# Optimization experiments

Measured on AMD Instinct MI355X. Metric: run time of the kernel, lower is better.

Reference implementation:

```python
import jax, jax.numpy as jnp
import numpy as np

EMBED_DIM = 1024
Q_DIM = 512
KV_DIM = 512
NUM_HEADS = 16
HEAD_DIM = EMBED_DIM // NUM_HEADS
EPS = 1e-5


def setup_inputs() -> dict:
    key = jax.random.key(0)
    ks = jax.random.split(key, 13)
    B, N1, N2 = 2, 2048, 2048
    s_q = 1.0 / np.sqrt(Q_DIM)
    s_kv = 1.0 / np.sqrt(KV_DIM)
    s_e = 1.0 / np.sqrt(EMBED_DIM)
    return {
        "query": jax.random.normal(ks[0], (B, N1, Q_DIM), jnp.float32),
        "key": jax.random.normal(ks[1], (B, N2, KV_DIM), jnp.float32),
        "value": jax.random.normal(ks[2], (B, N2, KV_DIM), jnp.float32),
        "Wq": jax.random.uniform(ks[3], (Q_DIM, EMBED_DIM), jnp.float32, -s_q, s_q),
        "bq": jax.random.uniform(ks[4], (EMBED_DIM,), jnp.float32, -s_q, s_q),
        "Wk": jax.random.uniform(ks[5], (KV_DIM, EMBED_DIM), jnp.float32, -s_kv, s_kv),
        "bk": jax.random.uniform(ks[6], (EMBED_DIM,), jnp.float32, -s_kv, s_kv),
        "Wv": jax.random.uniform(ks[7], (KV_DIM, EMBED_DIM), jnp.float32, -s_kv, s_kv),
        "bv": jax.random.uniform(ks[8], (EMBED_DIM,), jnp.float32, -s_kv, s_kv),
        "Wo": jax.random.uniform(ks[9], (EMBED_DIM, EMBED_DIM), jnp.float32, -s_e, s_e),
        "bo": jax.random.uniform(ks[10], (EMBED_DIM,), jnp.float32, -s_e, s_e),
        "gamma": jnp.ones((EMBED_DIM,), jnp.float32),
        "beta": jnp.zeros((EMBED_DIM,), jnp.float32),
    }


def reference(query, key, value, Wq, bq, Wk, bk, Wv, bv, Wo, bo, gamma, beta):
    B, N1, _ = query.shape
    _, N2, _ = key.shape
    scale = HEAD_DIM ** (-0.5)
    # projections -> [B, H, N, D]
    Q = (query @ Wq + bq).reshape(B, N1, NUM_HEADS, HEAD_DIM).transpose(0, 2, 1, 3)
    K = (key @ Wk + bk).reshape(B, N2, NUM_HEADS, HEAD_DIM).transpose(0, 2, 1, 3)
    V = (value @ Wv + bv).reshape(B, N2, NUM_HEADS, HEAD_DIM).transpose(0, 2, 1, 3)
    # full score matrix [B, H, N1, N2] (matches original eager attention)
    att = jnp.einsum("bhqd,bhkd->bhqk", Q, K) * scale
    att = jax.nn.softmax(att, axis=-1)
    # dropout is identity in eval mode
    out = jnp.einsum("bhqk,bhkd->bhqd", att, V)  # [B, H, N1, D]
    out = out.transpose(0, 2, 1, 3).reshape(B, N1, EMBED_DIM)
    out = out @ Wo + bo
    # LayerNorm
    mu = out.mean(-1, keepdims=True)
    var = ((out - mu) ** 2).mean(-1, keepdims=True)
    return (out - mu) * jax.lax.rsqrt(var + EPS) * gamma + beta
```

## Files before the change

kernel.cpp:

```cpp
#include <hip/hip_runtime.h>

typedef __bf16 bf16x8 __attribute__((ext_vector_type(8)));
typedef __bf16 bf16x4 __attribute__((ext_vector_type(4)));
typedef __bf16 bf16x2 __attribute__((ext_vector_type(2)));
typedef float f32x4 __attribute__((ext_vector_type(4)));
typedef unsigned short u16;
typedef unsigned int u32;

__device__ __forceinline__ f32x4 mfma16(bf16x8 a, bf16x8 b, f32x4 c) {
  return __builtin_amdgcn_mfma_f32_16x16x32_bf16(a, b, c, 0, 0, 0);
}

__device__ __forceinline__ void gload_lds16(const void* g, void* l) {
  __builtin_amdgcn_global_load_lds(
      (const __attribute__((address_space(1))) void*)g,
      (__attribute__((address_space(3))) void*)l, 16, 0, 0);
}

__device__ __forceinline__ void swap32(u32& a, u32& b) {
  asm volatile("v_permlane32_swap_b32 %0, %1" : "+v"(a), "+v"(b));
}
__device__ __forceinline__ void swap16(u32& a, u32& b) {
  asm volatile("v_permlane16_swap_b32 %0, %1" : "+v"(a), "+v"(b));
}

__device__ __forceinline__ u32 pkbf(float a, float b) {
  union { bf16x2 h; u32 w; } u;
  u.h[0] = (__bf16)a;
  u.h[1] = (__bf16)b;
  return u.w;
}

__global__ __launch_bounds__(256) void prep(const float4* __restrict__ qi,
                                            const float4* __restrict__ ki,
                                            const float4* __restrict__ vi,
                                            bf16x4* __restrict__ oq,
                                            bf16x4* __restrict__ ok,
                                            bf16x4* __restrict__ ov,
                                            const float* __restrict__ W0,
                                            const float* __restrict__ W1,
                                            const float* __restrict__ W2,
                                            const float* __restrict__ W3,
                                            u16* __restrict__ T0, u16* __restrict__ T1,
                                            u16* __restrict__ T2, u16* __restrict__ T3,
                                            int n4) {
  const int z = blockIdx.y;
  const int tid = threadIdx.x;
  if (z < 3) {
    int i = blockIdx.x * 256 + tid;
    if (i >= n4) return;
    const float4* in = z == 0 ? qi : z == 1 ? ki : vi;
    bf16x4* out = z == 0 ? oq : z == 1 ? ok : ov;
    float4 v = in[i];
    bf16x4 o;
    o[0] = (__bf16)v.x; o[1] = (__bf16)v.y; o[2] = (__bf16)v.z; o[3] = (__bf16)v.w;
    out[i] = o;
  } else {
    const int zz = z - 3;
    const int K = (zz == 3) ? 1024 : 512;
    const int nb = (K / 32) * 32;
    if (blockIdx.x >= nb) return;
    const float* W = zz == 0 ? W0 : zz == 1 ? W1 : zz == 2 ? W2 : W3;
    u16* Wt = zz == 0 ? T0 : zz == 1 ? T1 : zz == 2 ? T2 : T3;
    __shared__ float t[32][33];
    const int tx = tid & 31, ty = tid >> 5;
    const int n0 = (blockIdx.x & 31) * 32, k0 = (blockIdx.x >> 5) * 32;
#pragma unroll
    for (int i = 0; i < 4; ++i)
      t[ty + i * 8][tx] = W[(size_t)(k0 + ty + i * 8) * 1024 + n0 + tx];
    __syncthreads();
#pragma unroll
    for (int i = 0; i < 4; ++i)
      ((__bf16*)Wt)[(size_t)(n0 + ty + i * 8) * K + k0 + tx] = (__bf16)t[tx][ty + i * 8];
  }
}

template <int MODE, int DBUF>
__device__ __forceinline__ void gemm_body(const u16* __restrict__ A,
                                          const u16* __restrict__ Bt,
                                          const float* __restrict__ bias,
                                          void* __restrict__ Cout,
                                          int M, int N, int K, float scl) {
  constexpr int NB = DBUF ? 2 : 1;
  __shared__ __align__(16) u16 lA[NB][128 * 64];
  __shared__ __align__(16) u16 lB[NB][128 * 64];
  const int tid = threadIdx.x;
  const int w = tid >> 6, l = tid & 63;
  const int li = l & 15, lg = l >> 4;
  const int wm = w & 1, wn = w >> 1;
  const int bm = blockIdx.x * 128, bn = blockIdx.y * 128;

  f32x4 acc[4][4] = {};
  const int nk = K >> 6;

  auto stage = [&](int kt, int bufi) {
    const int k0 = kt << 6;
#pragma unroll
    for (int i = 0; i < 4; ++i) {
      const int c0 = (i * 4 + w) * 64;
      const int f = c0 + l;
      const int r = f >> 3, cs = (f & 7) ^ (r & 7);
      gload_lds16(A + (size_t)(bm + r) * K + k0 + cs * 8, &lA[bufi][c0 * 8]);
      gload_lds16(Bt + (size_t)(bn + r) * K + k0 + cs * 8, &lB[bufi][c0 * 8]);
    }
  };

  int cur = 0;
  if (DBUF) {
    stage(0, 0);
    __syncthreads();
  }

  for (int kt = 0; kt < nk; ++kt) {
    if (DBUF) {
      if (kt + 1 < nk) stage(kt + 1, cur ^ 1);
    } else {
      stage(kt, 0);
      __syncthreads();
    }
    bf16x8 af[4][2], bfr[4][2];
#pragma unroll
    for (int m = 0; m < 4; ++m) {
      const int row = wm * 64 + m * 16 + li;
#pragma unroll
      for (int kk = 0; kk < 2; ++kk) {
        const int kc = (lg + kk * 4) ^ (row & 7);
        af[m][kk] = *(const bf16x8*)&lA[cur][row * 64 + kc * 8];
      }
    }
#pragma unroll
    for (int n = 0; n < 4; ++n) {
      const int row = wn * 64 + n * 16 + li;
#pragma unroll
      for (int kk = 0; kk < 2; ++kk) {
        const int kc = (lg + kk * 4) ^ (row & 7);
        bfr[n][kk] = *(const bf16x8*)&lB[cur][row * 64 + kc * 8];
      }
    }
#pragma unroll
    for (int m = 0; m < 4; ++m)
#pragma unroll
      for (int n = 0; n < 4; ++n) {
        acc[m][n] = mfma16(af[m][0], bfr[n][0], acc[m][n]);
        acc[m][n] = mfma16(af[m][1], bfr[n][1], acc[m][n]);
      }
    __syncthreads();
    if (DBUF) cur ^= 1;
  }

#pragma unroll
  for (int m = 0; m < 4; ++m) {
    const int row0 = bm + wm * 64 + m * 16 + lg * 4;
#pragma unroll
    for (int n = 0; n < 4; ++n) {
      const int col = bn + wn * 64 + n * 16 + li;
      const float bv = bias[col];
      if (MODE == 2) {
        const int bq = row0 >> 11, kv = row0 & 2047;
        bf16x4 pk;
#pragma unroll
        for (int r = 0; r < 4; ++r) pk[r] = (__bf16)((acc[m][n][r] + bv) * scl);
        *(bf16x4*)&((u16*)Cout)[((size_t)(bq * 1024 + col)) * 2048 + kv] = pk;
      } else {
#pragma unroll
        for (int r = 0; r < 4; ++r) {
          float v = (acc[m][n][r] + bv) * scl;
          ((__bf16*)Cout)[(size_t)(row0 + r) * N + col] = (__bf16)v;
        }
      }
    }
  }
}

__global__ __launch_bounds__(256) void gemm_qkv(const u16* __restrict__ xq,
                                                const u16* __restrict__ xk,
                                                const u16* __restrict__ xv,
                                                const u16* __restrict__ wqt,
                                                const u16* __restrict__ wkt,
                                                const u16* __restrict__ wvt,
                                                const float* __restrict__ bq,
                                                const float* __restrict__ bk,
                                                const float* __restrict__ bv,
                                                u16* __restrict__ Qb, u16* __restrict__ Kb,
                                                u16* __restrict__ Vt, float qscale) {
  const int z = blockIdx.z;
  if (z == 0) {
    gemm_body<0, 0>(xq, wqt, bq, Qb, 4096, 1024, 512, qscale);
  } else if (z == 1) {
    gemm_body<0, 0>(xk, wkt, bk, Kb, 4096, 1024, 512, 1.0f);
  } else {
    gemm_body<2, 0>(xv, wvt, bv, Vt, 4096, 1024, 512, 1.0f);
  }
}

__global__ __launch_bounds__(512) void gemm_o8(const u16* __restrict__ A,
                                               const u16* __restrict__ Bt,
                                               const float* __restrict__ bias,
                                               u16* __restrict__ C) {
  constexpr int N = 1024, K = 1024;
  __shared__ __align__(16) u16 lA[2][128 * 64];
  __shared__ __align__(16) u16 lB[2][128 * 64];
  const int tid = threadIdx.x;
  const int w = tid >> 6, l = tid & 63;
  const int li = l & 15, lg = l >> 4;
  const int wm = w & 1, wn = w >> 1;
  const int bm = blockIdx.x * 128, bn = blockIdx.y * 128;

  f32x4 acc[4][2] = {};
  const int nk = K >> 6;

  auto stage = [&](int kt, int bufi) {
    const int k0 = kt << 6;
#pragma unroll
    for (int i = 0; i < 2; ++i) {
      const int c0 = (i * 8 + w) * 64;
      const int f = c0 + l;
      const int r = f >> 3, cs = (f & 7) ^ (r & 7);
      gload_lds16(A + (size_t)(bm + r) * K + k0 + cs * 8, &lA[bufi][c0 * 8]);
      gload_lds16(Bt + (size_t)(bn + r) * K + k0 + cs * 8, &lB[bufi][c0 * 8]);
    }
  };

  int cur = 0;
  stage(0, 0);
  __syncthreads();

  for (int kt = 0; kt < nk; ++kt) {
    if (kt + 1 < nk) stage(kt + 1, cur ^ 1);
    bf16x8 af[4][2], bfr[2][2];
#pragma unroll
    for (int m = 0; m < 4; ++m) {
      const int row = wm * 64 + m * 16 + li;
#pragma unroll
      for (int kk = 0; kk < 2; ++kk) {
        const int kc = (lg + kk * 4) ^ (row & 7);
        af[m][kk] = *(const bf16x8*)&lA[cur][row * 64 + kc * 8];
      }
    }
#pragma unroll
    for (int n = 0; n < 2; ++n) {
      const int row = wn * 32 + n * 16 + li;
#pragma unroll
      for (int kk = 0; kk < 2; ++kk) {
        const int kc = (lg + kk * 4) ^ (row & 7);
        bfr[n][kk] = *(const bf16x8*)&lB[cur][row * 64 + kc * 8];
      }
    }
#pragma unroll
    for (int m = 0; m < 4; ++m)
#pragma unroll
      for (int n = 0; n < 2; ++n) {
        acc[m][n] = mfma16(af[m][0], bfr[n][0], acc[m][n]);
        acc[m][n] = mfma16(af[m][1], bfr[n][1], acc[m][n]);
      }
    __syncthreads();
    cur ^= 1;
  }

#pragma unroll
  for (int m = 0; m < 4; ++m) {
    const int row0 = bm + wm * 64 + m * 16 + lg * 4;
#pragma unroll
    for (int n = 0; n < 2; ++n) {
      const int col = bn + wn * 32 + n * 16 + li;
      const float bv = bias[col];
#pragma unroll
      for (int r = 0; r < 4; ++r)
        ((__bf16*)C)[(size_t)(row0 + r) * N + col] = (__bf16)(acc[m][n][r] + bv);
    }
  }
}

__global__ __launch_bounds__(512, 4) void attn64(const u16* __restrict__ Qb,
                                                 const u16* __restrict__ Kb,
                                                 const u16* __restrict__ Vt,
                                                 u16* __restrict__ Opart,
                                                 float* __restrict__ Lpart,
                                                 int N1, int N2) {
  const int tid = threadIdx.x;
  const int w = tid >> 6, l = tid & 63;
  const int li = l & 15, lg = l >> 4;

  const int flat = blockIdx.x + 8 * (blockIdx.y + 16 * blockIdx.z);
  const int xcd = flat & 7, idx = flat >> 3;
  const int qb = idx & 7, rest = idx >> 3;
  const int h = 2 * xcd + (rest & 1);
  const int b = (rest >> 1) & 1;
  const int kvh = rest >> 2;
  const int q0 = qb * 256;

  __shared__ __align__(16) u16 lK[4][64 * 64];
  __shared__ __align__(16) u16 lV[4][64 * 64];

  bf16x8 qa[2][2];
#pragma unroll
  for (int s = 0; s < 2; ++s) {
    const size_t qoff = (size_t)(b * N1 + q0 + s * 128 + w * 16 + li) * 1024 + h * 64;
    qa[s][0] = *(const bf16x8*)&Qb[qoff + lg * 8];
    qa[s][1] = *(const bf16x8*)&Qb[qoff + 32 + lg * 8];
  }

  const u16* Kbase = Kb + (size_t)b * N2 * 1024 + h * 64;
  const u16* Vbase = Vt + (size_t)((b * 16 + h) * 64) * N2;

  const int sr = tid >> 3;
  const int sc = (tid & 7) ^ (sr & 7);

  f32x4 o[2][4] = {};
  float lsum0 = 0.f, lsum1 = 0.f;
  const int ca = lg ^ (li & 7), cb = (lg + 4) ^ (li & 7);

  auto stageK = [&](int t, int bufi) {
    gload_lds16(Kbase + (size_t)(t * 64 + sr) * 1024 + sc * 8, &lK[bufi][w * 512]);
  };
  auto stageV = [&](int t, int bufi) {
    gload_lds16(Vbase + (size_t)sr * N2 + t * 64 + sc * 8, &lV[bufi][w * 512]);
  };

  auto tile_body = [&](const u16* K_, const u16* V_) {
    float st0 = 0.f, st1 = 0.f;
    u32 u0[4][2], u1[4][2];
    __builtin_amdgcn_s_setprio(1);
#pragma unroll
    for (int n = 0; n < 4; ++n) {
      const int row = n * 16 + li;
      bf16x8 k0 = *(const bf16x8*)&K_[row * 64 + ca * 8];
      bf16x8 k1 = *(const bf16x8*)&K_[row * 64 + cb * 8];
      f32x4 a = {}, a2 = {};
      a = mfma16(k0, qa[0][0], a);
      a = mfma16(k1, qa[0][1], a);
      a2 = mfma16(k0, qa[1][0], a2);
      a2 = mfma16(k1, qa[1][1], a2);
      float p0 = __builtin_amdgcn_exp2f(a[0]);
      float p1 = __builtin_amdgcn_exp2f(a[1]);
      float p2 = __builtin_amdgcn_exp2f(a[2]);
      float p3 = __builtin_amdgcn_exp2f(a[3]);
      st0 += (p0 + p1) + (p2 + p3);
      u0[n][0] = pkbf(p0, p1);
      u0[n][1] = pkbf(p2, p3);
      float r0 = __builtin_amdgcn_exp2f(a2[0]);
      float r1 = __builtin_amdgcn_exp2f(a2[1]);
      float r2 = __builtin_amdgcn_exp2f(a2[2]);
      float r3 = __builtin_amdgcn_exp2f(a2[3]);
      st1 += (r0 + r1) + (r2 + r3);
      u1[n][0] = pkbf(r0, r1);
      u1[n][1] = pkbf(r2, r3);
    }
    __builtin_amdgcn_s_setprio(0);
    lsum0 += st0;
    lsum1 += st1;

#pragma unroll
    for (int c = 0; c < 2; ++c) {
      swap32(u0[0][c], u0[1][c]); swap32(u0[2][c], u0[3][c]);
      swap32(u1[0][c], u1[1][c]); swap32(u1[2][c], u1[3][c]);
    }
#pragma unroll
    for (int c = 0; c < 2; ++c) {
      swap16(u0[0][c], u0[1][c]); swap16(u0[2][c], u0[3][c]);
      swap16(u1[0][c], u1[1][c]); swap16(u1[2][c], u1[3][c]);
    }

    __builtin_amdgcn_s_setprio(1);
#pragma unroll
    for (int ks = 0; ks < 2; ++ks) {
      union { u32 w4[4]; bf16x8 v; } f0, f1;
      f0.w4[0] = u0[2 * ks][0]; f0.w4[1] = u0[2 * ks][1];
      f0.w4[2] = u0[2 * ks + 1][0]; f0.w4[3] = u0[2 * ks + 1][1];
      f1.w4[0] = u1[2 * ks][0]; f1.w4[1] = u1[2 * ks][1];
      f1.w4[2] = u1[2 * ks + 1][0]; f1.w4[3] = u1[2 * ks + 1][1];
#pragma unroll
      for (int dt = 0; dt < 4; ++dt) {
        const int row = dt * 16 + li;
        const int c = (lg + ks * 4) ^ (li & 7);
        const bf16x8 vf = *(const bf16x8*)&V_[row * 64 + c * 8];
        o[0][dt] = mfma16(vf, f0.v, o[0][dt]);
        o[1][dt] = mfma16(vf, f1.v, o[1][dt]);
      }
    }
    __builtin_amdgcn_s_setprio(0);
  };

  const int t0 = kvh * 16;

  stageK(t0, 0); stageV(t0, 0);
  stageK(t0 + 1, 1); stageV(t0 + 1, 1);
  __syncthreads();

  for (int tt = 0; tt < 16; tt += 2) {
    const int t = t0 + tt;
    if (tt + 2 < 16) { stageK(t + 2, (tt + 2) & 3); stageV(t + 2, (tt + 2) & 3); }
    if (tt + 3 < 16) { stageK(t + 3, (tt + 3) & 3); stageV(t + 3, (tt + 3) & 3); }
    tile_body(lK[tt & 3], lV[tt & 3]);
    tile_body(lK[(tt + 1) & 3], lV[(tt + 1) & 3]);
    __syncthreads();
  }

  lsum0 += __shfl_xor(lsum0, 16, 64);
  lsum0 += __shfl_xor(lsum0, 32, 64);
  lsum1 += __shfl_xor(lsum1, 16, 64);
  lsum1 += __shfl_xor(lsum1, 32, 64);

  u16* Op = Opart + (size_t)kvh * 4096 * 1024;
#pragma unroll
  for (int s = 0; s < 2; ++s) {
    const int qrow = b * N1 + q0 + s * 128 + w * 16 + li;
    const size_t orow = (size_t)qrow * 1024 + h * 64;
#pragma unroll
    for (int dt = 0; dt < 4; ++dt) {
      bf16x4 pk;
#pragma unroll
      for (int r = 0; r < 4; ++r) pk[r] = (__bf16)o[s][dt][r];
      *(bf16x4*)&Op[orow + dt * 16 + lg * 4] = pk;
    }
    if (lg == 0)
      Lpart[(size_t)kvh * 4096 * 16 + (size_t)qrow * 16 + h] = (s == 0 ? lsum0 : lsum1);
  }
}

__global__ __launch_bounds__(256) void combine(const u16* __restrict__ Opart,
                                               const float* __restrict__ Lpart,
                                               u16* __restrict__ ao) {
  const int row = blockIdx.x;
  const int tid = threadIdx.x;
  const int h = tid >> 4;
  const float l = Lpart[(size_t)row * 16 + h] + Lpart[4096 * 16 + (size_t)row * 16 + h];
  const float inv = 1.f / l;
  const size_t off = (size_t)row * 1024 + tid * 4;
  const bf16x4 a = *(const bf16x4*)&Opart[off];
  const bf16x4 b = *(const bf16x4*)&Opart[(size_t)4096 * 1024 + off];
  bf16x4 o;
#pragma unroll
  for (int j = 0; j < 4; ++j) o[j] = (__bf16)(((float)a[j] + (float)b[j]) * inv);
  *(bf16x4*)&ao[off] = o;
}

__global__ __launch_bounds__(256) void lnorm(const u16* __restrict__ X,
                                             const float* __restrict__ gamma,
                                             const float* __restrict__ beta,
                                             float* __restrict__ out) {
  const int row = blockIdx.x;
  const int tid = threadIdx.x;
  const bf16x4 xv = ((const bf16x4*)(X + (size_t)row * 1024))[tid];
  float4 v;
  v.x = (float)xv[0]; v.y = (float)xv[1]; v.z = (float)xv[2]; v.w = (float)xv[3];
  float s = v.x + v.y + v.z + v.w;
  float sq = v.x * v.x + v.y * v.y + v.z * v.z + v.w * v.w;
#pragma unroll
  for (int d = 1; d < 64; d <<= 1) {
    s += __shfl_xor(s, d, 64);
    sq += __shfl_xor(sq, d, 64);
  }
  __shared__ float red[8];
  const int w = tid >> 6, l = tid & 63;
  if (l == 0) { red[w] = s; red[4 + w] = sq; }
  __syncthreads();
  s = red[0] + red[1] + red[2] + red[3];
  sq = red[4] + red[5] + red[6] + red[7];
  const float mu = s * (1.f / 1024.f);
  const float var = sq * (1.f / 1024.f) - mu * mu;
  const float rstd = rsqrtf(var + 1e-5f);
  const float4 g = ((const float4*)gamma)[tid];
  const float4 bb = ((const float4*)beta)[tid];
  float4 o;
  o.x = (v.x - mu) * rstd * g.x + bb.x;
  o.y = (v.y - mu) * rstd * g.y + bb.y;
  o.z = (v.z - mu) * rstd * g.z + bb.z;
  o.w = (v.w - mu) * rstd * g.w + bb.w;
  ((float4*)(out + (size_t)row * 1024))[tid] = o;
}

extern "C" void kernel_launch(void* const* d_in, const int* in_sizes, int n_in,
                              void* d_out, int out_size, void* d_ws, size_t ws_size,
                              hipStream_t stream) {
  const float* query = (const float*)d_in[0];
  const float* key_ = (const float*)d_in[1];
  const float* value = (const float*)d_in[2];
  const float* Wq = (const float*)d_in[3];
  const float* bq = (const float*)d_in[4];
  const float* Wk = (const float*)d_in[5];
  const float* bk = (const float*)d_in[6];
  const float* Wv = (const float*)d_in[7];
  const float* bv = (const float*)d_in[8];
  const float* Wo = (const float*)d_in[9];
  const float* bo = (const float*)d_in[10];
  const float* gamma = (const float*)d_in[11];
  const float* beta = (const float*)d_in[12];

  constexpr int B = 2, N1 = 2048, N2 = 2048, E = 1024, QKD = 512;
  constexpr int M = B * N1;
  const float QSCALE = 0.125f * 1.4426950408889634f;

  char* p = (char*)d_ws;
  auto alloc = [&](size_t bytes) {
    char* r = p;
    p += (bytes + 255) & ~(size_t)255;
    return r;
  };
  u16* xq = (u16*)alloc((size_t)M * QKD * 2);
  u16* xk = (u16*)alloc((size_t)M * QKD * 2);
  u16* xv = (u16*)alloc((size_t)M * QKD * 2);
  u16* wqt = (u16*)alloc((size_t)E * QKD * 2);
  u16* wkt = (u16*)alloc((size_t)E * QKD * 2);
  u16* wvt = (u16*)alloc((size_t)E * QKD * 2);
  u16* wot = (u16*)alloc((size_t)E * E * 2);
  u16* Qb = (u16*)alloc((size_t)M * E * 2);
  u16* Kb = (u16*)alloc((size_t)M * E * 2);
  u16* Vt = (u16*)alloc((size_t)M * E * 2);
  u16* ao = (u16*)alloc((size_t)M * E * 2);
  u16* ao2 = (u16*)alloc((size_t)M * E * 2);
  u16* Opart = (u16*)alloc((size_t)2 * M * E * 2);
  float* Lpart = (float*)alloc((size_t)2 * M * 16 * 4);

  const int n4 = M * QKD / 4;
  prep<<<dim3((n4 + 255) / 256, 7), 256, 0, stream>>>(
      (const float4*)query, (const float4*)key_, (const float4*)value,
      (bf16x4*)xq, (bf16x4*)xk, (bf16x4*)xv,
      Wq, Wk, Wv, Wo, wqt, wkt, wvt, wot, n4);

  gemm_qkv<<<dim3(M / 128, E / 128, 3), 256, 0, stream>>>(
      xq, xk, xv, wqt, wkt, wvt, bq, bk, bv, Qb, Kb, Vt, QSCALE);

  attn64<<<dim3(8, 16, 4), 512, 0, stream>>>(Qb, Kb, Vt, Opart, Lpart, N1, N2);

  combine<<<M, 256, 0, stream>>>(Opart, Lpart, ao);

  gemm_o8<<<dim3(M / 128, E / 128), 512, 0, stream>>>(ao, wot, bo, ao2);

  lnorm<<<M, 256, 0, stream>>>(ao2, gamma, beta, (float*)d_out);
}
```

Before: 103.6 us.

## Fuse split-KV combine into output GEMM and use 8-wave double-buffered QKV GEMM

The separate combine kernel is removed. The output-projection GEMM now loads both partial attention outputs and their softmax denominators, sums and normalizes them in registers, and writes the A tile into LDS while B is still staged asynchronously. The QKV projection GEMM moves to 512 threads with 8 waves and double-buffered LDS, matching the output GEMM. This saves one launch and a full round trip through the intermediate activation buffer. In exchange it adds register pressure and global-to-register loads on the output GEMM's A path.

```diff
diff --git a/kernel.cpp b/kernel.cpp
--- a/kernel.cpp
+++ b/kernel.cpp
@@ -75,29 +75,28 @@
   }
 }
 
-template <int MODE, int DBUF>
-__device__ __forceinline__ void gemm_body(const u16* __restrict__ A,
-                                          const u16* __restrict__ Bt,
-                                          const float* __restrict__ bias,
-                                          void* __restrict__ Cout,
-                                          int M, int N, int K, float scl) {
-  constexpr int NB = DBUF ? 2 : 1;
-  __shared__ __align__(16) u16 lA[NB][128 * 64];
-  __shared__ __align__(16) u16 lB[NB][128 * 64];
+template <int MODE>
+__device__ __forceinline__ void gemm8_body(const u16* __restrict__ A,
+                                           const u16* __restrict__ Bt,
+                                           const float* __restrict__ bias,
+                                           u16* __restrict__ Cout,
+                                           int N, int K, float scl) {
+  __shared__ __align__(16) u16 lA[2][128 * 64];
+  __shared__ __align__(16) u16 lB[2][128 * 64];
   const int tid = threadIdx.x;
   const int w = tid >> 6, l = tid & 63;
   const int li = l & 15, lg = l >> 4;
   const int wm = w & 1, wn = w >> 1;
   const int bm = blockIdx.x * 128, bn = blockIdx.y * 128;
 
-  f32x4 acc[4][4] = {};
+  f32x4 acc[4][2] = {};
   const int nk = K >> 6;
 
   auto stage = [&](int kt, int bufi) {
     const int k0 = kt << 6;
 #pragma unroll
-    for (int i = 0; i < 4; ++i) {
-      const int c0 = (i * 4 + w) * 64;
+    for (int i = 0; i < 2; ++i) {
+      const int c0 = (i * 8 + w) * 64;
       const int f = c0 + l;
       const int r = f >> 3, cs = (f & 7) ^ (r & 7);
       gload_lds16(A + (size_t)(bm + r) * K + k0 + cs * 8, &lA[bufi][c0 * 8]);
@@ -106,19 +105,12 @@
   };
 
   int cur = 0;
-  if (DBUF) {
-    stage(0, 0);
-    __syncthreads();
-  }
+  stage(0, 0);
+  __syncthreads();
 
   for (int kt = 0; kt < nk; ++kt) {
-    if (DBUF) {
-      if (kt + 1 < nk) stage(kt + 1, cur ^ 1);
-    } else {
-      stage(kt, 0);
-      __syncthreads();
-    }
-    bf16x8 af[4][2], bfr[4][2];
+    if (kt + 1 < nk) stage(kt + 1, cur ^ 1);
+    bf16x8 af[4][2], bfr[2][2];
 #pragma unroll
     for (int m = 0; m < 4; ++m) {
       const int row = wm * 64 + m * 16 + li;
@@ -129,8 +121,8 @@
       }
     }
 #pragma unroll
-    for (int n = 0; n < 4; ++n) {
-      const int row = wn * 64 + n * 16 + li;
+    for (int n = 0; n < 2; ++n) {
+      const int row = wn * 32 + n * 16 + li;
 #pragma unroll
       for (int kk = 0; kk < 2; ++kk) {
         const int kc = (lg + kk * 4) ^ (row & 7);
@@ -140,60 +132,61 @@
 #pragma unroll
     for (int m = 0; m < 4; ++m)
 #pragma unroll
-      for (int n = 0; n < 4; ++n) {
+      for (int n = 0; n < 2; ++n) {
         acc[m][n] = mfma16(af[m][0], bfr[n][0], acc[m][n]);
         acc[m][n] = mfma16(af[m][1], bfr[n][1], acc[m][n]);
       }
     __syncthreads();
-    if (DBUF) cur ^= 1;
+    cur ^= 1;
   }
 
 #pragma unroll
   for (int m = 0; m < 4; ++m) {
     const int row0 = bm + wm * 64 + m * 16 + lg * 4;
 #pragma unroll
-    for (int n = 0; n < 4; ++n) {
-      const int col = bn + wn * 64 + n * 16 + li;
+    for (int n = 0; n < 2; ++n) {
+      const int col = bn + wn * 32 + n * 16 + li;
       const float bv = bias[col];
       if (MODE == 2) {
         const int bq = row0 >> 11, kv = row0 & 2047;
         bf16x4 pk;
 #pragma unroll
         for (int r = 0; r < 4; ++r) pk[r] = (__bf16)((acc[m][n][r] + bv) * scl);
-        *(bf16x4*)&((u16*)Cout)[((size_t)(bq * 1024 + col)) * 2048 + kv] = pk;
+        *(bf16x4*)&Cout[((size_t)(bq * 1024 + col)) * 2048 + kv] = pk;
       } else {
 #pragma unroll
-        for (int r = 0; r < 4; ++r) {
-          float v = (acc[m][n][r] + bv) * scl;
-          ((__bf16*)Cout)[(size_t)(row0 + r) * N + col] = (__bf16)v;
-        }
-      }
-    }
-  }
-}
-
-__global__ __launch_bounds__(256) void gemm_qkv(const u16* __restrict__ xq,
-                                                const u16* __restrict__ xk,
-                                                const u16* __restrict__ xv,
-                                                const u16* __restrict__ wqt,
-                                                const u16* __restrict__ wkt,
-                                                const u16* __restrict__ wvt,
-                                                const float* __restrict__ bq,
-                                                const float* __restrict__ bk,
-                                                const float* __restrict__ bv,
-                                                u16* __restrict__ Qb, u16* __restrict__ Kb,
-                                                u16* __restrict__ Vt, float qscale) {
+        for (int r = 0; r < 4; ++r)
+          ((__bf16*)Cout)[(size_t)(row0 + r) * N + col] = (__bf16)((acc[m][n][r] + bv) * scl);
+      }
+    }
+  }
+}
+
+__global__ __launch_bounds__(512) void gemm_qkv8(const u16* __restrict__ xq,
+                                                 const u16* __restrict__ xk,
+                                                 const u16* __restrict__ xv,
+                                                 const u16* __restrict__ wqt,
+                                                 const u16* __restrict__ wkt,
+                                                 const u16* __restrict__ wvt,
+                                                 const float* __restrict__ bq,
+                                                 const float* __restrict__ bk,
+                                                 const float* __restrict__ bv,
+                                                 u16* __restrict__ Qb, u16* __restrict__ Kb,
+                                                 u16* __restrict__ Vt, float qscale) {
   const int z = blockIdx.z;
   if (z == 0) {
-    gemm_body<0, 0>(xq, wqt, bq, Qb, 4096, 1024, 512, qscale);
+    gemm8_body<0>(xq, wqt, bq, Qb, 1024, 512, qscale);
   } else if (z == 1) {
-    gemm_body<0, 0>(xk, wkt, bk, Kb, 4096, 1024, 512, 1.0f);
+    gemm8_body<0>(xk, wkt, bk, Kb, 1024, 512, 1.0f);
   } else {
-    gemm_body<2, 0>(xv, wvt, bv, Vt, 4096, 1024, 512, 1.0f);
-  }
-}
-
-__global__ __launch_bounds__(512) void gemm_o8(const u16* __restrict__ A,
+    gemm8_body<2>(xv, wvt, bv, Vt, 1024, 512, 1.0f);
+  }
+}
+
+__global__ __launch_bounds__(512) void gemm_oc(const u16* __restrict__ Op0,
+                                               const u16* __restrict__ Op1,
+                                               const float* __restrict__ Lp0,
+                                               const float* __restrict__ Lp1,
                                                const u16* __restrict__ Bt,
                                                const float* __restrict__ bias,
                                                u16* __restrict__ C) {
@@ -209,24 +202,55 @@
   f32x4 acc[4][2] = {};
   const int nk = K >> 6;
 
-  auto stage = [&](int kt, int bufi) {
+  bf16x8 a0[2], a1[2];
+  float inv[2];
+
+  auto loadA = [&](int kt) {
     const int k0 = kt << 6;
 #pragma unroll
     for (int i = 0; i < 2; ++i) {
       const int c0 = (i * 8 + w) * 64;
       const int f = c0 + l;
       const int r = f >> 3, cs = (f & 7) ^ (r & 7);
-      gload_lds16(A + (size_t)(bm + r) * K + k0 + cs * 8, &lA[bufi][c0 * 8]);
+      const int row = bm + r;
+      a0[i] = *(const bf16x8*)&Op0[(size_t)row * 1024 + k0 + cs * 8];
+      a1[i] = *(const bf16x8*)&Op1[(size_t)row * 1024 + k0 + cs * 8];
+      inv[i] = 1.f / (Lp0[row * 16 + kt] + Lp1[row * 16 + kt]);
+    }
+  };
+  auto writeA = [&](int bufi) {
+#pragma unroll
+    for (int i = 0; i < 2; ++i) {
+      const int c0 = (i * 8 + w) * 64;
+      bf16x8 o;
+#pragma unroll
+      for (int j = 0; j < 8; ++j)
+        o[j] = (__bf16)(((float)a0[i][j] + (float)a1[i][j]) * inv[i]);
+      *(bf16x8*)&lA[bufi][c0 * 8 + l * 8] = o;
+    }
+  };
+  auto stageB = [&](int kt, int bufi) {
+    const int k0 = kt << 6;
+#pragma unroll
+    for (int i = 0; i < 2; ++i) {
+      const int c0 = (i * 8 + w) * 64;
+      const int f = c0 + l;
+      const int r = f >> 3, cs = (f & 7) ^ (r & 7);
       gload_lds16(Bt + (size_t)(bn + r) * K + k0 + cs * 8, &lB[bufi][c0 * 8]);
     }
   };
 
   int cur = 0;
-  stage(0, 0);
+  loadA(0);
+  stageB(0, 0);
+  writeA(0);
   __syncthreads();
 
   for (int kt = 0; kt < nk; ++kt) {
-    if (kt + 1 < nk) stage(kt + 1, cur ^ 1);
+    if (kt + 1 < nk) {
+      loadA(kt + 1);
+      stageB(kt + 1, cur ^ 1);
+    }
     bf16x8 af[4][2], bfr[2][2];
 #pragma unroll
     for (int m = 0; m < 4; ++m) {
@@ -253,6 +277,7 @@
         acc[m][n] = mfma16(af[m][0], bfr[n][0], acc[m][n]);
         acc[m][n] = mfma16(af[m][1], bfr[n][1], acc[m][n]);
       }
+    if (kt + 1 < nk) writeA(cur ^ 1);
     __syncthreads();
     cur ^= 1;
   }
@@ -418,23 +443,6 @@
   }
 }
 
-__global__ __launch_bounds__(256) void combine(const u16* __restrict__ Opart,
-                                               const float* __restrict__ Lpart,
-                                               u16* __restrict__ ao) {
-  const int row = blockIdx.x;
-  const int tid = threadIdx.x;
-  const int h = tid >> 4;
-  const float l = Lpart[(size_t)row * 16 + h] + Lpart[4096 * 16 + (size_t)row * 16 + h];
-  const float inv = 1.f / l;
-  const size_t off = (size_t)row * 1024 + tid * 4;
-  const bf16x4 a = *(const bf16x4*)&Opart[off];
-  const bf16x4 b = *(const bf16x4*)&Opart[(size_t)4096 * 1024 + off];
-  bf16x4 o;
-#pragma unroll
-  for (int j = 0; j < 4; ++j) o[j] = (__bf16)(((float)a[j] + (float)b[j]) * inv);
-  *(bf16x4*)&ao[off] = o;
-}
-
 __global__ __launch_bounds__(256) void lnorm(const u16* __restrict__ X,
                                              const float* __restrict__ gamma,
                                              const float* __restrict__ beta,
@@ -507,7 +515,6 @@
   u16* Qb = (u16*)alloc((size_t)M * E * 2);
   u16* Kb = (u16*)alloc((size_t)M * E * 2);
   u16* Vt = (u16*)alloc((size_t)M * E * 2);
-  u16* ao = (u16*)alloc((size_t)M * E * 2);
   u16* ao2 = (u16*)alloc((size_t)M * E * 2);
   u16* Opart = (u16*)alloc((size_t)2 * M * E * 2);
   float* Lpart = (float*)alloc((size_t)2 * M * 16 * 4);
@@ -518,14 +525,14 @@
       (bf16x4*)xq, (bf16x4*)xk, (bf16x4*)xv,
       Wq, Wk, Wv, Wo, wqt, wkt, wvt, wot, n4);
 
-  gemm_qkv<<<dim3(M / 128, E / 128, 3), 256, 0, stream>>>(
+  gemm_qkv8<<<dim3(M / 128, E / 128, 3), 512, 0, stream>>>(
       xq, xk, xv, wqt, wkt, wvt, bq, bk, bv, Qb, Kb, Vt, QSCALE);
 
   attn64<<<dim3(8, 16, 4), 512, 0, stream>>>(Qb, Kb, Vt, Opart, Lpart, N1, N2);
 
-  combine<<<M, 256, 0, stream>>>(Opart, Lpart, ao);
-
-  gemm_o8<<<dim3(M / 128, E / 128), 512, 0, stream>>>(ao, wot, bo, ao2);
+  gemm_oc<<<dim3(M / 128, E / 128), 512, 0, stream>>>(
+      Opart, Opart + (size_t)M * E, Lpart, Lpart + (size_t)M * 16,
+      wot, bo, ao2);
 
   lnorm<<<M, 256, 0, stream>>>(ao2, gamma, beta, (float*)d_out);
 }
```

Measured after the change: 114.4 us. +10.4%, slower.
